# Performance work log

Hardware: AMD Instinct MI355X
Metric: run time of the kernel (lower is better)

## Reference

```python
import jax, jax.numpy as jnp
import numpy as np

# DCNv2 (ModulatedDeformConvPack) config, matching init_kwargs
STRIDE, PAD, DIL = 1, 1, 1
DG = 8            # deformable_groups
KH = KW = 3
CIN, COUT = 64, 64
B, H, W = 2, 128, 128


def setup_inputs() -> dict:
    key = jax.random.key(0)
    k1, k2, k3, k4 = jax.random.split(key, 4)
    x = jax.random.normal(k1, (B, CIN, H, W), dtype=jnp.float32)
    # conv_offset: Conv2d(CIN, DG*3*KH*KW, 3, stride=1, pad=1). Zero-init in the
    # original; use small random weights so offsets/mask are non-trivial.
    conv_offset_w = jax.random.normal(k2, (DG * 3 * KH * KW, CIN, KH, KW), dtype=jnp.float32) * 0.01
    conv_offset_b = jax.random.normal(k3, (DG * 3 * KH * KW,), dtype=jnp.float32) * 0.01
    n = CIN * KH * KW
    stdv = 1.0 / np.sqrt(n)
    weight = jax.random.uniform(k4, (COUT, CIN, KH, KW), dtype=jnp.float32, minval=-stdv, maxval=stdv)
    bias = jnp.zeros((COUT,), dtype=jnp.float32)
    return {"x": x, "conv_offset_w": conv_offset_w, "conv_offset_b": conv_offset_b,
            "weight": weight, "bias": bias}


def _dcn_v2(x, conv_offset_w, conv_offset_b, weight, bias):
    Bn, Cin, Hh, Ww = x.shape
    Cout, _, kh, kw = weight.shape
    K = kh * kw
    cpg = Cin // DG  # channels per deformable group

    # offset/mask predictor conv (standard conv)
    out = jax.lax.conv_general_dilated(
        x, conv_offset_w, window_strides=(STRIDE, STRIDE),
        padding=[(PAD, PAD), (PAD, PAD)], rhs_dilation=(DIL, DIL),
        dimension_numbers=("NCHW", "OIHW", "NCHW")) + conv_offset_b[None, :, None, None]
    o1, o2, mask = jnp.split(out, 3, axis=1)
    offset = jnp.concatenate([o1, o2], axis=1)          # (B, 2*DG*K, Ho, Wo)
    Ho, Wo = offset.shape[2], offset.shape[3]
    # CUDA kernel reads offset channels as [dg, K, (y, x)]
    off = offset.reshape(Bn, DG, K, 2, Ho, Wo)
    off_y = off[:, :, :, 0]                              # (B, DG, K, Ho, Wo)
    off_x = off[:, :, :, 1]
    mask = jax.nn.sigmoid(mask).reshape(Bn, DG, K, Ho, Wo)

    ki = (jnp.arange(K) // kw).astype(x.dtype)           # tap row index
    kj = (jnp.arange(K) % kw).astype(x.dtype)            # tap col index
    base_y = jnp.arange(Ho, dtype=x.dtype) * STRIDE - PAD
    base_x = jnp.arange(Wo, dtype=x.dtype) * STRIDE - PAD
    py = off_y + base_y[None, None, None, :, None] + (ki * DIL)[None, None, :, None, None]
    px = off_x + base_x[None, None, None, None, :] + (kj * DIL)[None, None, :, None, None]

    y0 = jnp.floor(py)
    x0 = jnp.floor(px)
    ly = py - y0
    lx = px - x0
    y0i = y0.astype(jnp.int32)
    x0i = x0.astype(jnp.int32)

    xg = x.reshape(Bn, DG, cpg, Hh, Ww)
    bi = jnp.arange(Bn)[:, None, None, None, None]
    gi = jnp.arange(DG)[None, :, None, None, None]

    def gather(yi, xi):
        # zero padding outside the image (matches CUDA corner validity checks)
        valid = (yi >= 0) & (yi <= Hh - 1) & (xi >= 0) & (xi <= Ww - 1)
        yc = jnp.clip(yi, 0, Hh - 1)
        xc = jnp.clip(xi, 0, Ww - 1)
        v = xg[bi, gi, :, yc, xc]                        # (B, DG, K, Ho, Wo, cpg)
        return v * valid[..., None].astype(x.dtype)

    v00 = gather(y0i, x0i)
    v01 = gather(y0i, x0i + 1)
    v10 = gather(y0i + 1, x0i)
    v11 = gather(y0i + 1, x0i + 1)
    hy, hx = 1.0 - ly, 1.0 - lx
    val = ((hy * hx)[..., None] * v00 + (hy * lx)[..., None] * v01 +
           (ly * hx)[..., None] * v10 + (ly * lx)[..., None] * v11)

    col = val * mask[..., None]                          # modulated columns
    wr = weight.reshape(Cout, DG, cpg, K)
    y = jnp.einsum('bgkhwc,ogck->bohw', col, wr) + bias[None, :, None, None]
    return y


def reference(x, conv_offset_w, conv_offset_b, weight, bias):
    return _dcn_v2(x, conv_offset_w, conv_offset_b, weight, bias)
```

## Files before the change

### kernel.cpp

```cpp
#include <hip/hip_runtime.h>
#include <hip/hip_fp16.h>

constexpr int BB = 2;
constexpr int CINc = 64;
constexpr int HWc = 128 * 128;
constexpr int OCOFFc = 216;
constexpr int XP = 130;

constexpr size_t XT_BYTES  = (size_t)BB * 8 * XP * XP * 8 * 2;
constexpr size_t WB1_OFF   = XT_BYTES;
constexpr size_t WB1_BYTES = (size_t)9 * 8 * 256 * 8 * 2;
constexpr size_t WM_OFF    = WB1_OFF + WB1_BYTES;
constexpr size_t WM_BYTES  = (size_t)8 * 12 * 64 * 8 * 2;
constexpr size_t WS_NEEDED = WM_OFF + WM_BYTES;

typedef _Float16 f16x8 __attribute__((ext_vector_type(8)));
typedef float    f32x4 __attribute__((ext_vector_type(4)));

__global__ void prep_all(const float* __restrict__ x, const float* __restrict__ w_off,
                         const float* __restrict__ weight,
                         __half* __restrict__ xT, __half* __restrict__ wB1,
                         __half* __restrict__ wM) {
    int bid = blockIdx.x;
    if (bid < 1024) {
        int site = bid * 256 + threadIdx.x;
        int pix = site & (HWc - 1);
        int bdg = site >> 14;
        int dg = bdg & 7, b = bdg >> 3;
        int y = pix >> 7, xc = pix & 127;
        const float* xp = x + (size_t)(b * CINc + dg * 8) * HWc + pix;
        __half2 h0 = __halves2half2(__float2half(xp[0 * HWc]), __float2half(xp[1 * HWc]));
        __half2 h1 = __halves2half2(__float2half(xp[2 * HWc]), __float2half(xp[3 * HWc]));
        __half2 h2 = __halves2half2(__float2half(xp[4 * HWc]), __float2half(xp[5 * HWc]));
        __half2 h3 = __halves2half2(__float2half(xp[6 * HWc]), __float2half(xp[7 * HWc]));
        __half2* o = reinterpret_cast<__half2*>(
            xT + (((size_t)(b * 8 + dg) * XP + y + 1) * XP + xc + 1) * 8);
        o[0] = h0; o[1] = h1; o[2] = h2; o[3] = h3;
        return;
    }
    int idx = (bid - 1024) * 256 + threadIdx.x;
    if (idx < 9 * 8 * 256 * 8) {
        int ci = idx & 7;
        int oc = (idx >> 3) & 255;
        int c  = (idx >> 11) & 7;
        int tap = idx >> 14;
        float v = (oc < OCOFFc) ? w_off[oc * 576 + (c * 8 + ci) * 9 + tap] : 0.f;
        wB1[idx] = __float2half(v);
    } else if (idx < 9 * 8 * 256 * 8 + 8 * 12 * 64 * 8) {
        int j = idx - 9 * 8 * 256 * 8;
        int c = j & 7;
        int oc = (j >> 3) & 63;
        int tg = j >> 9;
        int tap = tg % 12;
        int dg = tg / 12;
        float v = (tap < 9) ? weight[oc * 576 + (dg * 8 + c) * 9 + tap] : 0.f;
        wM[j] = __float2half(v);
    } else {
        int j2 = idx - (9 * 8 * 256 * 8 + 8 * 12 * 64 * 8);
        if (j2 < 16 * 516) {
            int plane = j2 / 516;
            int p = j2 - plane * 516;
            int y, xx;
            if (p < 130)      { y = 0;           xx = p; }
            else if (p < 260) { y = 129;         xx = p - 130; }
            else if (p < 388) { y = 1 + p - 260; xx = 0; }
            else              { y = 1 + p - 388; xx = 129; }
            uint4 z = {0u, 0u, 0u, 0u};
            *reinterpret_cast<uint4*>(xT + (((size_t)plane * XP + y) * XP + xx) * 8) = z;
        }
    }
}

#define DCN_IC(D_, S_, BF, G, W, ACT)                                          \
  {                                                                            \
    const int dci_ = (D_);                                                     \
    if (ACT) {                                                                 \
      _Pragma("unroll")                                                        \
      for (int n_ = 0; n_ < 4; ++n_)                                           \
        BF[n_] = *reinterpret_cast<const f16x8*>(                              \
            wM + (size_t)((dci_ * 12 + (S_) * 4 + lh) * 64 + n_ * 16 + l15) * 8); \
      const int kg_ = (S_) * 4 + lh;                                           \
      if ((S_) < 2 || lh == 0) {                                               \
        uint2 ov_ = *reinterpret_cast<const uint2*>(                           \
            offsb + ((size_t)(dci_ * 128 + px)) * 36 + kg_ * 4);               \
        __half2 p0_ = *reinterpret_cast<const __half2*>(&ov_.x);               \
        __half2 p1_ = *reinterpret_cast<const __half2*>(&ov_.y);               \
        float oy_ = __half2float(__low2half(p0_));                             \
        float ox_ = __half2float(__high2half(p0_));                            \
        float mk_ = __half2float(__low2half(p1_));                             \
        const int ki_ = kg_ / 3, kj_ = kg_ - ki_ * 3;                          \
        float sy_ = oy_ + (float)(gy - 1 + ki_);                               \
        float sx_ = ox_ + (float)(gx - 1 + kj_);                               \
        float y0f_ = floorf(sy_), x0f_ = floorf(sx_);                          \
        int iy0_ = (int)y0f_, ix0_ = (int)x0f_;                                \
        float ly_ = sy_ - y0f_, lx_ = sx_ - x0f_;                              \
        float hy_ = 1.f - ly_, hx_ = 1.f - lx_;                                \
        float vy0_ = ((unsigned)iy0_ < 128u) ? 1.f : 0.f;                      \
        float vy1_ = ((unsigned)(iy0_ + 1) < 128u) ? 1.f : 0.f;                \
        float vx0_ = ((unsigned)ix0_ < 128u) ? 1.f : 0.f;                      \
        float vx1_ = ((unsigned)(ix0_ + 1) < 128u) ? 1.f : 0.f;                \
        W[0] = __floats2half2_rn(hy_ * hx_ * vy0_ * vx0_ * mk_,                \
                                 hy_ * lx_ * vy0_ * vx1_ * mk_);               \
        W[1] = __floats2half2_rn(ly_ * hx_ * vy1_ * vx0_ * mk_,                \
                                 ly_ * lx_ * vy1_ * vx1_ * mk_);               \
        int y0c_ = min(max(iy0_, 0), 127), y1c_ = min(max(iy0_ + 1, 0), 127);  \
        int x0c_ = min(max(ix0_, 0), 127), x1c_ = min(max(ix0_ + 1, 0), 127);  \
        const __half* xb_ = xT + (size_t)(b * 8 + dci_) * XP * XP * 8;         \
        G[0] = *reinterpret_cast<const float4*>(xb_ + ((size_t)(y0c_ + 1) * XP + x0c_ + 1) * 8); \
        G[1] = *reinterpret_cast<const float4*>(xb_ + ((size_t)(y0c_ + 1) * XP + x1c_ + 1) * 8); \
        G[2] = *reinterpret_cast<const float4*>(xb_ + ((size_t)(y1c_ + 1) * XP + x0c_ + 1) * 8); \
        G[3] = *reinterpret_cast<const float4*>(xb_ + ((size_t)(y1c_ + 1) * XP + x1c_ + 1) * 8); \
      } else {                                                                 \
        const float4 z4_ = {0.f, 0.f, 0.f, 0.f};                               \
        W[0] = __float2half2_rn(0.f); W[1] = __float2half2_rn(0.f);            \
        G[0] = z4_; G[1] = z4_; G[2] = z4_; G[3] = z4_;                        \
      }                                                                        \
    } else {                                                                   \
      const float4 z4_ = {0.f, 0.f, 0.f, 0.f};                                 \
      const f16x8 zf_ = {0, 0, 0, 0, 0, 0, 0, 0};                              \
      W[0] = __float2half2_rn(0.f); W[1] = __float2half2_rn(0.f);              \
      G[0] = z4_; G[1] = z4_; G[2] = z4_; G[3] = z4_;                          \
      BF[0] = zf_; BF[1] = zf_; BF[2] = zf_; BF[3] = zf_;                      \
    }                                                                          \
  }

#define DCN_CC(BF, G, W)                                                       \
  {                                                                            \
    __half2 W00_ = __half2half2(__low2half(W[0]));                             \
    __half2 W01_ = __half2half2(__high2half(W[0]));                            \
    __half2 W10_ = __half2half2(__low2half(W[1]));                             \
    __half2 W11_ = __half2half2(__high2half(W[1]));                            \
    const __half2* a00_ = reinterpret_cast<const __half2*>(&G[0]);             \
    const __half2* a01_ = reinterpret_cast<const __half2*>(&G[1]);             \
    const __half2* a10_ = reinterpret_cast<const __half2*>(&G[2]);             \
    const __half2* a11_ = reinterpret_cast<const __half2*>(&G[3]);             \
    __align__(16) __half2 rr_[4];                                              \
    _Pragma("unroll")                                                          \
    for (int cc_ = 0; cc_ < 4; ++cc_)                                          \
      rr_[cc_] = __hfma2(a00_[cc_], W00_,                                      \
                 __hfma2(a01_[cc_], W01_,                                      \
                 __hfma2(a10_[cc_], W10_, __hmul2(a11_[cc_], W11_))));         \
    f16x8 af_ = *reinterpret_cast<const f16x8*>(rr_);                          \
    _Pragma("unroll")                                                          \
    for (int n_ = 0; n_ < 4; ++n_)                                             \
      acc2[n_] = __builtin_amdgcn_mfma_f32_16x16x32_f16(                       \
          af_, BF[n_], acc2[n_], 0, 0, 0);                                     \
  }

__global__ __launch_bounds__(512, 2) void dcn_fused_k(
        const __half* __restrict__ xT, const __half* __restrict__ wB1,
        const float* __restrict__ cob, const __half* __restrict__ wM,
        const float* __restrict__ bias, float* __restrict__ out) {
    __shared__ __half xs[1440 * 8];
    __shared__ __half offsb[8 * 128 * 36];
    const int tid = threadIdx.x;
    const int fid = blockIdx.x + (blockIdx.y << 3) + (blockIdx.z << 7);
    const int vid = ((fid & 7) << 5) + (fid >> 3);
    const int bx = vid & 7;
    const int by = (vid >> 3) & 15;
    const int b  = vid >> 7;

    #pragma unroll
    for (int it = 0; it < 3; ++it) {
        int idx = tid + it * 512;
        if (idx < 1440) {
            int yl = idx / 144;
            int rem = idx - yl * 144;
            int cl = rem >> 3, sl = rem & 7;
            int dg = sl ^ (cl & 7);
            float4 v = *reinterpret_cast<const float4*>(
                xT + (((size_t)(b * 8 + dg) * XP + by * 8 + yl) * XP + bx * 16 + cl) * 8);
            *reinterpret_cast<float4*>(xs + idx * 8) = v;
        }
    }
    __syncthreads();

    const int lane = tid & 63;
    const int wid = tid >> 6;
    const int l15 = lane & 15, lh = lane >> 4;

    {
        const int wr = wid & 1;
        const int wc = wid >> 1;
        f32x4 acc[4][4];
        const f32x4 zero = {0.f, 0.f, 0.f, 0.f};
        #pragma unroll
        for (int ty = 0; ty < 4; ++ty)
            #pragma unroll
            for (int ot = 0; ot < 4; ++ot) acc[ty][ot] = zero;

        #pragma unroll 3
        for (int tap = 0; tap < 9; ++tap) {
            const int r = tap / 3, s = tap - r * 3;
            const int j = l15 + s;
            #pragma unroll
            for (int h = 0; h < 2; ++h) {
                const int c = h * 4 + lh;
                const int sl = c ^ (j & 7);
                f16x8 af[4], bf[4];
                #pragma unroll
                for (int ot = 0; ot < 4; ++ot) {
                    int oc = wc * 64 + ot * 16 + l15;
                    bf[ot] = *reinterpret_cast<const f16x8*>(
                        wB1 + (size_t)(((tap * 8 + c) * 256 + oc)) * 8);
                }
                #pragma unroll
                for (int ty = 0; ty < 4; ++ty) {
                    int row = wr * 4 + ty + r;
                    af[ty] = *reinterpret_cast<const f16x8*>(xs + (row * 18 + j) * 64 + sl * 8);
                }
                #pragma unroll
                for (int ty = 0; ty < 4; ++ty)
                    #pragma unroll
                    for (int ot = 0; ot < 4; ++ot)
                        acc[ty][ot] = __builtin_amdgcn_mfma_f32_16x16x32_f16(
                            af[ty], bf[ot], acc[ty][ot], 0, 0, 0);
            }
        }

        #pragma unroll
        for (int ot = 0; ot < 4; ++ot) {
            int oc = wc * 64 + ot * 16 + l15;
            if (oc < OCOFFc) {
                float bi = cob[oc];
                bool sig = (oc >= 144);
                int dg, k, comp;
                if (oc < 144) { dg = oc / 18; int rem = oc - dg * 18; k = rem >> 1; comp = rem & 1; }
                else          { int mm = oc - 144; dg = mm / 9; k = mm - dg * 9; comp = 2; }
                #pragma unroll
                for (int ty = 0; ty < 4; ++ty) {
                    int pxw = (wr * 4 + ty) * 16 + lh * 4;
                    float v0 = acc[ty][ot][0] + bi, v1 = acc[ty][ot][1] + bi;
                    float v2 = acc[ty][ot][2] + bi, v3 = acc[ty][ot][3] + bi;
                    if (sig) {
                        v0 = 1.f / (1.f + __expf(-v0)); v1 = 1.f / (1.f + __expf(-v1));
                        v2 = 1.f / (1.f + __expf(-v2)); v3 = 1.f / (1.f + __expf(-v3));
                    }
                    size_t base = (size_t)(dg * 128) * 36 + k * 4 + comp;
                    offsb[base + (size_t)(pxw + 0) * 36] = __float2half(v0);
                    offsb[base + (size_t)(pxw + 1) * 36] = __float2half(v1);
                    offsb[base + (size_t)(pxw + 2) * 36] = __float2half(v2);
                    offsb[base + (size_t)(pxw + 3) * 36] = __float2half(v3);
                }
            }
        }
    }
    __syncthreads();

    const int px = wid * 16 + l15;
    const int gy = by * 8 + wid;
    const int gx = bx * 16 + l15;

    f32x4 acc2[4];
    const f32x4 zero2 = {0.f, 0.f, 0.f, 0.f};
    #pragma unroll
    for (int n = 0; n < 4; ++n) acc2[n] = zero2;

    f16x8 bfX[4], bfY[4];
    float4 gX[4], gY[4];
    __half2 wX[2], wY[2];

    DCN_IC(0, 0, bfX, gX, wX, true);
    #pragma unroll 1
    for (int dp = 0; dp < 4; ++dp) {
        const int d0 = dp * 2;
        DCN_IC(d0,     1, bfY, gY, wY, true);     DCN_CC(bfX, gX, wX);
        DCN_IC(d0,     2, bfX, gX, wX, true);     DCN_CC(bfY, gY, wY);
        DCN_IC(d0 + 1, 0, bfY, gY, wY, true);     DCN_CC(bfX, gX, wX);
        DCN_IC(d0 + 1, 1, bfX, gX, wX, true);     DCN_CC(bfY, gY, wY);
        DCN_IC(d0 + 1, 2, bfY, gY, wY, true);     DCN_CC(bfX, gX, wX);
        DCN_IC(d0 + 2, 0, bfX, gX, wX, dp < 3);   DCN_CC(bfY, gY, wY);
    }

    #pragma unroll
    for (int n = 0; n < 4; ++n) {
        int oc = n * 16 + l15;
        float bi = bias[oc];
        float4 v = make_float4(acc2[n][0] + bi, acc2[n][1] + bi,
                               acc2[n][2] + bi, acc2[n][3] + bi);
        *reinterpret_cast<float4*>(
            out + (size_t)(b * 64 + oc) * HWc + gy * 128 + bx * 16 + lh * 4) = v;
    }
}

extern "C" void kernel_launch(void* const* d_in, const int* in_sizes, int n_in,
                              void* d_out, int out_size, void* d_ws, size_t ws_size,
                              hipStream_t stream) {
    const float* x      = (const float*)d_in[0];
    const float* w_off  = (const float*)d_in[1];
    const float* cob    = (const float*)d_in[2];
    const float* weight = (const float*)d_in[3];
    const float* bias   = (const float*)d_in[4];
    float* out = (float*)d_out;
    if (ws_size < WS_NEEDED) return;

    char* ws = (char*)d_ws;
    __half* xT  = (__half*)ws;
    __half* wB1 = (__half*)(ws + WB1_OFF);
    __half* wM  = (__half*)(ws + WM_OFF);

    prep_all<<<1825, 256, 0, stream>>>(x, w_off, weight, xT, wB1, wM);
    dcn_fused_k<<<dim3(8, 16, 2), 512, 0, stream>>>(xT, wB1, cob, wM, bias, out);
}
```

Before: 38.06 us.

## Pack DCN weights densely without tap padding and stage half in LDS

Repacks the modulated-conv weights from 12 padded tap slots per group (8x12) into 72 dense slots, so every 4-lane-group K-step does useful work and the zero-padded slots are gone. The sampling loop becomes 18 fully unrolled steps instead of 24. The first 36 weight slots are copied into shared memory at block start and read from there, while the rest still come from global memory. This costs more LDS per block, which may affect occupancy at 2 blocks per CU, and the larger unrolled code may raise register pressure.

```diff
diff --git a/kernel.cpp b/kernel.cpp
--- a/kernel.cpp
+++ b/kernel.cpp
@@ -11,7 +11,7 @@
 constexpr size_t WB1_OFF   = XT_BYTES;
 constexpr size_t WB1_BYTES = (size_t)9 * 8 * 256 * 8 * 2;
 constexpr size_t WM_OFF    = WB1_OFF + WB1_BYTES;
-constexpr size_t WM_BYTES  = (size_t)8 * 12 * 64 * 8 * 2;
+constexpr size_t WM_BYTES  = (size_t)72 * 64 * 8 * 2;
 constexpr size_t WS_NEEDED = WM_OFF + WM_BYTES;
 
 typedef _Float16 f16x8 __attribute__((ext_vector_type(8)));
@@ -20,7 +20,7 @@
 __global__ void prep_all(const float* __restrict__ x, const float* __restrict__ w_off,
                          const float* __restrict__ weight,
                          __half* __restrict__ xT, __half* __restrict__ wB1,
-                         __half* __restrict__ wM) {
+                         __half* __restrict__ wM2) {
     int bid = blockIdx.x;
     if (bid < 1024) {
         int site = bid * 256 + threadIdx.x;
@@ -46,17 +46,16 @@
         int tap = idx >> 14;
         float v = (oc < OCOFFc) ? w_off[oc * 576 + (c * 8 + ci) * 9 + tap] : 0.f;
         wB1[idx] = __float2half(v);
-    } else if (idx < 9 * 8 * 256 * 8 + 8 * 12 * 64 * 8) {
+    } else if (idx < 9 * 8 * 256 * 8 + 72 * 64 * 8) {
         int j = idx - 9 * 8 * 256 * 8;
-        int c = j & 7;
+        int ci = j & 7;
         int oc = (j >> 3) & 63;
-        int tg = j >> 9;
-        int tap = tg % 12;
-        int dg = tg / 12;
-        float v = (tap < 9) ? weight[oc * 576 + (dg * 8 + c) * 9 + tap] : 0.f;
-        wM[j] = __float2half(v);
+        int slot = j >> 9;
+        int dg = slot / 9;
+        int tap = slot - dg * 9;
+        wM2[j] = __float2half(weight[oc * 576 + (dg * 8 + ci) * 9 + tap]);
     } else {
-        int j2 = idx - (9 * 8 * 256 * 8 + 8 * 12 * 64 * 8);
+        int j2 = idx - (9 * 8 * 256 * 8 + 72 * 64 * 8);
         if (j2 < 16 * 516) {
             int plane = j2 / 516;
             int p = j2 - plane * 516;
@@ -71,57 +70,51 @@
     }
 }
 
-#define DCN_IC(D_, S_, BF, G, W, ACT)                                          \
+#define DCN_IC(CC_, BF, G, W, LDSW)                                            \
   {                                                                            \
-    const int dci_ = (D_);                                                     \
-    if (ACT) {                                                                 \
+    const int slot_ = (CC_) * 4 + lh;                                          \
+    if (LDSW) {                                                                \
       _Pragma("unroll")                                                        \
       for (int n_ = 0; n_ < 4; ++n_)                                           \
         BF[n_] = *reinterpret_cast<const f16x8*>(                              \
-            wM + (size_t)((dci_ * 12 + (S_) * 4 + lh) * 64 + n_ * 16 + l15) * 8); \
-      const int kg_ = (S_) * 4 + lh;                                           \
-      if ((S_) < 2 || lh == 0) {                                               \
-        uint2 ov_ = *reinterpret_cast<const uint2*>(                           \
-            offsb + ((size_t)(dci_ * 128 + px)) * 36 + kg_ * 4);               \
-        __half2 p0_ = *reinterpret_cast<const __half2*>(&ov_.x);               \
-        __half2 p1_ = *reinterpret_cast<const __half2*>(&ov_.y);               \
-        float oy_ = __half2float(__low2half(p0_));                             \
-        float ox_ = __half2float(__high2half(p0_));                            \
-        float mk_ = __half2float(__low2half(p1_));                             \
-        const int ki_ = kg_ / 3, kj_ = kg_ - ki_ * 3;                          \
-        float sy_ = oy_ + (float)(gy - 1 + ki_);                               \
-        float sx_ = ox_ + (float)(gx - 1 + kj_);                               \
-        float y0f_ = floorf(sy_), x0f_ = floorf(sx_);                          \
-        int iy0_ = (int)y0f_, ix0_ = (int)x0f_;                                \
-        float ly_ = sy_ - y0f_, lx_ = sx_ - x0f_;                              \
-        float hy_ = 1.f - ly_, hx_ = 1.f - lx_;                                \
-        float vy0_ = ((unsigned)iy0_ < 128u) ? 1.f : 0.f;                      \
-        float vy1_ = ((unsigned)(iy0_ + 1) < 128u) ? 1.f : 0.f;                \
-        float vx0_ = ((unsigned)ix0_ < 128u) ? 1.f : 0.f;                      \
-        float vx1_ = ((unsigned)(ix0_ + 1) < 128u) ? 1.f : 0.f;                \
-        W[0] = __floats2half2_rn(hy_ * hx_ * vy0_ * vx0_ * mk_,                \
-                                 hy_ * lx_ * vy0_ * vx1_ * mk_);               \
-        W[1] = __floats2half2_rn(ly_ * hx_ * vy1_ * vx0_ * mk_,                \
-                                 ly_ * lx_ * vy1_ * vx1_ * mk_);               \
-        int y0c_ = min(max(iy0_, 0), 127), y1c_ = min(max(iy0_ + 1, 0), 127);  \
-        int x0c_ = min(max(ix0_, 0), 127), x1c_ = min(max(ix0_ + 1, 0), 127);  \
-        const __half* xb_ = xT + (size_t)(b * 8 + dci_) * XP * XP * 8;         \
-        G[0] = *reinterpret_cast<const float4*>(xb_ + ((size_t)(y0c_ + 1) * XP + x0c_ + 1) * 8); \
-        G[1] = *reinterpret_cast<const float4*>(xb_ + ((size_t)(y0c_ + 1) * XP + x1c_ + 1) * 8); \
-        G[2] = *reinterpret_cast<const float4*>(xb_ + ((size_t)(y1c_ + 1) * XP + x0c_ + 1) * 8); \
-        G[3] = *reinterpret_cast<const float4*>(xb_ + ((size_t)(y1c_ + 1) * XP + x1c_ + 1) * 8); \
-      } else {                                                                 \
-        const float4 z4_ = {0.f, 0.f, 0.f, 0.f};                               \
-        W[0] = __float2half2_rn(0.f); W[1] = __float2half2_rn(0.f);            \
-        G[0] = z4_; G[1] = z4_; G[2] = z4_; G[3] = z4_;                        \
-      }                                                                        \
+            wMl + ((size_t)slot_ * 64 + n_ * 16 + l15) * 8);                   \
     } else {                                                                   \
-      const float4 z4_ = {0.f, 0.f, 0.f, 0.f};                                 \
-      const f16x8 zf_ = {0, 0, 0, 0, 0, 0, 0, 0};                              \
-      W[0] = __float2half2_rn(0.f); W[1] = __float2half2_rn(0.f);              \
-      G[0] = z4_; G[1] = z4_; G[2] = z4_; G[3] = z4_;                          \
-      BF[0] = zf_; BF[1] = zf_; BF[2] = zf_; BF[3] = zf_;                      \
+      _Pragma("unroll")                                                        \
+      for (int n_ = 0; n_ < 4; ++n_)                                           \
+        BF[n_] = *reinterpret_cast<const f16x8*>(                              \
+            wM2 + ((size_t)slot_ * 64 + n_ * 16 + l15) * 8);                   \
     }                                                                          \
+    const int dgc_ = slot_ / 9;                                                \
+    const int tap_ = slot_ - dgc_ * 9;                                         \
+    uint2 ov_ = *reinterpret_cast<const uint2*>(                               \
+        offsb + ((size_t)(dgc_ * 128 + px)) * 36 + tap_ * 4);                  \
+    __half2 p0_ = *reinterpret_cast<const __half2*>(&ov_.x);                   \
+    __half2 p1_ = *reinterpret_cast<const __half2*>(&ov_.y);                   \
+    float oy_ = __half2float(__low2half(p0_));                                 \
+    float ox_ = __half2float(__high2half(p0_));                                \
+    float mk_ = __half2float(__low2half(p1_));                                 \
+    const int ki_ = tap_ / 3, kj_ = tap_ - ki_ * 3;                            \
+    float sy_ = oy_ + (float)(gy - 1 + ki_);                                   \
+    float sx_ = ox_ + (float)(gx - 1 + kj_);                                   \
+    float y0f_ = floorf(sy_), x0f_ = floorf(sx_);                              \
+    int iy0_ = (int)y0f_, ix0_ = (int)x0f_;                                    \
+    float ly_ = sy_ - y0f_, lx_ = sx_ - x0f_;                                  \
+    float hy_ = 1.f - ly_, hx_ = 1.f - lx_;                                    \
+    float vy0_ = ((unsigned)iy0_ < 128u) ? 1.f : 0.f;                          \
+    float vy1_ = ((unsigned)(iy0_ + 1) < 128u) ? 1.f : 0.f;                    \
+    float vx0_ = ((unsigned)ix0_ < 128u) ? 1.f : 0.f;                          \
+    float vx1_ = ((unsigned)(ix0_ + 1) < 128u) ? 1.f : 0.f;                    \
+    W[0] = __floats2half2_rn(hy_ * hx_ * vy0_ * vx0_ * mk_,                    \
+                             hy_ * lx_ * vy0_ * vx1_ * mk_);                   \
+    W[1] = __floats2half2_rn(ly_ * hx_ * vy1_ * vx0_ * mk_,                    \
+                             ly_ * lx_ * vy1_ * vx1_ * mk_);                   \
+    int y0c_ = min(max(iy0_, 0), 127), y1c_ = min(max(iy0_ + 1, 0), 127);      \
+    int x0c_ = min(max(ix0_, 0), 127), x1c_ = min(max(ix0_ + 1, 0), 127);      \
+    const __half* xb_ = xT + (size_t)(b * 8 + dgc_) * XP * XP * 8;             \
+    G[0] = *reinterpret_cast<const float4*>(xb_ + ((size_t)(y0c_ + 1) * XP + x0c_ + 1) * 8); \
+    G[1] = *reinterpret_cast<const float4*>(xb_ + ((size_t)(y0c_ + 1) * XP + x1c_ + 1) * 8); \
+    G[2] = *reinterpret_cast<const float4*>(xb_ + ((size_t)(y1c_ + 1) * XP + x0c_ + 1) * 8); \
+    G[3] = *reinterpret_cast<const float4*>(xb_ + ((size_t)(y1c_ + 1) * XP + x1c_ + 1) * 8); \
   }
 
 #define DCN_CC(BF, G, W)                                                       \
@@ -149,10 +142,11 @@
 
 __global__ __launch_bounds__(512, 2) void dcn_fused_k(
         const __half* __restrict__ xT, const __half* __restrict__ wB1,
-        const float* __restrict__ cob, const __half* __restrict__ wM,
+        const float* __restrict__ cob, const __half* __restrict__ wM2,
         const float* __restrict__ bias, float* __restrict__ out) {
     __shared__ __half xs[1440 * 8];
     __shared__ __half offsb[8 * 128 * 36];
+    __shared__ __half wMl[36 * 64 * 8];
     const int tid = threadIdx.x;
     const int fid = blockIdx.x + (blockIdx.y << 3) + (blockIdx.z << 7);
     const int vid = ((fid & 7) << 5) + (fid >> 3);
@@ -172,6 +166,13 @@
                 xT + (((size_t)(b * 8 + dg) * XP + by * 8 + yl) * XP + bx * 16 + cl) * 8);
             *reinterpret_cast<float4*>(xs + idx * 8) = v;
         }
+    }
+    #pragma unroll
+    for (int i = 0; i < 5; ++i) {
+        int idx = tid + i * 512;
+        if (idx < 2304)
+            *reinterpret_cast<float4*>(wMl + (size_t)idx * 8) =
+                *reinterpret_cast<const float4*>(wM2 + (size_t)idx * 8);
     }
     __syncthreads();
 
@@ -260,17 +261,25 @@
     float4 gX[4], gY[4];
     __half2 wX[2], wY[2];
 
-    DCN_IC(0, 0, bfX, gX, wX, true);
-    #pragma unroll 1
-    for (int dp = 0; dp < 4; ++dp) {
-        const int d0 = dp * 2;
-        DCN_IC(d0,     1, bfY, gY, wY, true);     DCN_CC(bfX, gX, wX);
-        DCN_IC(d0,     2, bfX, gX, wX, true);     DCN_CC(bfY, gY, wY);
-        DCN_IC(d0 + 1, 0, bfY, gY, wY, true);     DCN_CC(bfX, gX, wX);
-        DCN_IC(d0 + 1, 1, bfX, gX, wX, true);     DCN_CC(bfY, gY, wY);
-        DCN_IC(d0 + 1, 2, bfY, gY, wY, true);     DCN_CC(bfX, gX, wX);
-        DCN_IC(d0 + 2, 0, bfX, gX, wX, dp < 3);   DCN_CC(bfY, gY, wY);
-    }
+    DCN_IC(0,  bfX, gX, wX, true);
+    DCN_IC(1,  bfY, gY, wY, true);   DCN_CC(bfX, gX, wX);
+    DCN_IC(2,  bfX, gX, wX, true);   DCN_CC(bfY, gY, wY);
+    DCN_IC(3,  bfY, gY, wY, true);   DCN_CC(bfX, gX, wX);
+    DCN_IC(4,  bfX, gX, wX, true);   DCN_CC(bfY, gY, wY);
+    DCN_IC(5,  bfY, gY, wY, true);   DCN_CC(bfX, gX, wX);
+    DCN_IC(6,  bfX, gX, wX, true);   DCN_CC(bfY, gY, wY);
+    DCN_IC(7,  bfY, gY, wY, true);   DCN_CC(bfX, gX, wX);
+    DCN_IC(8,  bfX, gX, wX, true);   DCN_CC(bfY, gY, wY);
+    DCN_IC(9,  bfY, gY, wY, false);  DCN_CC(bfX, gX, wX);
+    DCN_IC(10, bfX, gX, wX, false);  DCN_CC(bfY, gY, wY);
+    DCN_IC(11, bfY, gY, wY, false);  DCN_CC(bfX, gX, wX);
+    DCN_IC(12, bfX, gX, wX, false);  DCN_CC(bfY, gY, wY);
+    DCN_IC(13, bfY, gY, wY, false);  DCN_CC(bfX, gX, wX);
+    DCN_IC(14, bfX, gX, wX, false);  DCN_CC(bfY, gY, wY);
+    DCN_IC(15, bfY, gY, wY, false);  DCN_CC(bfX, gX, wX);
+    DCN_IC(16, bfX, gX, wX, false);  DCN_CC(bfY, gY, wY);
+    DCN_IC(17, bfY, gY, wY, false);  DCN_CC(bfX, gX, wX);
+    DCN_CC(bfY, gY, wY);
 
     #pragma unroll
     for (int n = 0; n < 4; ++n) {
@@ -297,8 +306,8 @@
     char* ws = (char*)d_ws;
     __half* xT  = (__half*)ws;
     __half* wB1 = (__half*)(ws + WB1_OFF);
-    __half* wM  = (__half*)(ws + WM_OFF);
-
-    prep_all<<<1825, 256, 0, stream>>>(x, w_off, weight, xT, wB1, wM);
-    dcn_fused_k<<<dim3(8, 16, 2), 512, 0, stream>>>(xT, wB1, cob, wM, bias, out);
+    __half* wM2 = (__half*)(ws + WM_OFF);
+
+    prep_all<<<1777, 256, 0, stream>>>(x, w_off, weight, xT, wB1, wM2);
+    dcn_fused_k<<<dim3(8, 16, 2), 512, 0, stream>>>(xT, wB1, cob, wM2, bias, out);
 }
```

New measurement: 34.05 us (median of 2 runs). 10.5% less time.
